# Performance work log

Measured on AMD Instinct MI355X. Metric: run time of the kernel, lower is better.

The kernel has to match this reference:

```python
import jax, jax.numpy as jnp
import numpy as np

NUM_HEADS = 12


def setup_inputs() -> dict:
    key = jax.random.key(0)
    ks = jax.random.split(key, 9)
    B, T, C = 4, 2048, 768
    s = 1.0 / np.sqrt(C)
    return {
        "x": jax.random.normal(ks[0], (B, T, C), dtype=jnp.float32),
        "wq": jax.random.normal(ks[1], (C, C), dtype=jnp.float32) * s,
        "bq": jnp.zeros((C,), dtype=jnp.float32),
        "wk": jax.random.normal(ks[2], (C, C), dtype=jnp.float32) * s,
        "bk": jnp.zeros((C,), dtype=jnp.float32),
        "wv": jax.random.normal(ks[3], (C, C), dtype=jnp.float32) * s,
        "bv": jnp.zeros((C,), dtype=jnp.float32),
        "wo": jax.random.normal(ks[4], (C, C), dtype=jnp.float32) * s,
        "bo": jnp.zeros((C,), dtype=jnp.float32),
    }


def reference(x, wq, bq, wk, bk, wv, bv, wo, bo):
    B, T, C = x.shape
    H = NUM_HEADS
    D = C // H
    scale = D ** -0.5
    # projections: weights stored as [in, out] so y = x @ w + b
    q = (x @ wq + bq).reshape(B, T, H, D).transpose(0, 2, 1, 3)  # [B,H,T,D]
    k = (x @ wk + bk).reshape(B, T, H, D).transpose(0, 2, 1, 3)
    v = (x @ wv + bv).reshape(B, T, H, D).transpose(0, 2, 1, 3)
    scores = jnp.einsum("bhqd,bhkd->bhqk", q, k) * scale  # [B,H,T,T]
    probs = jax.nn.softmax(scores, axis=-1)
    out = jnp.einsum("bhqk,bhkd->bhqd", probs, v)  # [B,H,T,D]
    out = out.transpose(0, 2, 1, 3).reshape(B, T, C)
    return out @ wo + bo
```

## Files before the change

kernel.cpp:

```cpp
#include <hip/hip_runtime.h>
#include <math.h>

#define NB 4
#define T_SEQ 2048
#define C_DIM 768
#define NH 12
#define HD 64
#define M_TOK (NB * T_SEQ)
#define NE ((size_t)M_TOK * C_DIM)
#define WE ((size_t)C_DIM * C_DIM)
#define QSCALE 0.18033688011112042f

typedef short bf16x8 __attribute__((ext_vector_type(8)));
typedef float f32x4 __attribute__((ext_vector_type(4)));
typedef unsigned short u16x4 __attribute__((ext_vector_type(4)));
typedef unsigned short u16x8 __attribute__((ext_vector_type(8)));
typedef unsigned short ushort_t;

__device__ __forceinline__ unsigned short f2bf(float x) {
    unsigned u = __float_as_uint(x);
    u += 0x7FFFu + ((u >> 16) & 1u);
    return (unsigned short)(u >> 16);
}
__device__ __forceinline__ float bf2f(unsigned short h) {
    return __uint_as_float(((unsigned)h) << 16);
}
__device__ __forceinline__ int sw128(int row, int bytecol) {
    return row * 128 + (bytecol ^ ((row & 7) << 4));
}
__device__ __forceinline__ void gload16(const ushort_t* gp, ushort_t* lp) {
    __builtin_amdgcn_global_load_lds(
        (const __attribute__((address_space(1))) unsigned int*)(const void*)gp,
        (__attribute__((address_space(3))) unsigned int*)(void*)lp, 16, 0, 0);
}

__global__ __launch_bounds__(256) void prep(
    const float* __restrict__ X,
    const float* __restrict__ wq, const float* __restrict__ wk,
    const float* __restrict__ wv, const float* __restrict__ wo,
    ushort_t* __restrict__ XH, ushort_t* __restrict__ Wbase)
{
    __shared__ float T[64][65];
    const int tid = threadIdx.x;
    const int bid = blockIdx.x;

    if (bid < 3072) {
        const size_t i = ((size_t)bid * 256 + tid) * 8;
        const float4 f0 = *(const float4*)&X[i];
        const float4 f1 = *(const float4*)&X[i + 4];
        const float xs[8] = {f0.x, f0.y, f0.z, f0.w, f1.x, f1.y, f1.z, f1.w};
        u16x8 h;
        #pragma unroll
        for (int j = 0; j < 8; ++j) h[j] = f2bf(xs[j]);
        *(u16x8*)&XH[i] = h;
        return;
    }

    const int r_ = bid - 3072;
    const int z = r_ / 144;
    const int rem = r_ % 144;
    const int ti = rem / 12, nj = rem % 12;
    const float* W = (z == 0) ? wq : (z == 1) ? wk : (z == 2) ? wv : wo;
    ushort_t* TH = Wbase + (size_t)z * 2 * WE;
    ushort_t* TL = TH + WE;
    {
        const int r = tid >> 2, cq = (tid & 3) * 16;
        #pragma unroll
        for (int j = 0; j < 4; ++j) {
            const float4 f = *(const float4*)&W[(size_t)(ti * 64 + r) * C_DIM + nj * 64 + cq + j * 4];
            T[r][cq + j * 4 + 0] = f.x;
            T[r][cq + j * 4 + 1] = f.y;
            T[r][cq + j * 4 + 2] = f.z;
            T[r][cq + j * 4 + 3] = f.w;
        }
    }
    __syncthreads();
    {
        const int n = tid >> 2, kq = (tid & 3) * 16;
        u16x8 h0, h1, l0, l1;
        #pragma unroll
        for (int j = 0; j < 8; ++j) {
            float v = T[kq + j][n];
            unsigned short hh = f2bf(v);
            h0[j] = hh; l0[j] = f2bf(v - bf2f(hh));
            v = T[kq + 8 + j][n];
            hh = f2bf(v);
            h1[j] = hh; l1[j] = f2bf(v - bf2f(hh));
        }
        const size_t o = (size_t)(nj * 64 + n) * C_DIM + ti * 64 + kq;
        *(u16x8*)&TH[o] = h0; *(u16x8*)&TH[o + 8] = h1;
        *(u16x8*)&TL[o] = l0; *(u16x8*)&TL[o + 8] = l1;
    }
}

__global__ __launch_bounds__(256, 4) void gemm_qkv(
    const ushort_t* __restrict__ XH,
    const ushort_t* __restrict__ WQH, const ushort_t* __restrict__ WKH,
    const ushort_t* __restrict__ WVH,
    const float* __restrict__ bq, const float* __restrict__ bk,
    const float* __restrict__ bv,
    ushort_t* __restrict__ Qo, ushort_t* __restrict__ Ko, ushort_t* __restrict__ VTo)
{
    __shared__ ushort_t TA[2][128 * 32];
    __shared__ ushort_t TB[2][128 * 32];

    const int tid = threadIdx.x, lane = tid & 63, w = tid >> 6;
    const int l15 = lane & 15, g = lane >> 4;
    const int wr = w >> 1, wc = w & 1;

    int bid = (int)blockIdx.x;
    bid = (bid & 7) * 144 + (bid >> 3);
    const int bm = bid / 18, bn = bid % 18;
    const int wsel = bn / 6, bnw = bn % 6;

    const ushort_t* BH = (wsel == 0) ? WQH : (wsel == 1) ? WKH : WVH;
    const float* bias = (wsel == 0) ? bq : (wsel == 1) ? bk : bv;

    f32x4 acc[4][4];
    #pragma unroll
    for (int m = 0; m < 4; ++m)
        #pragma unroll
        for (int n = 0; n < 4; ++n) acc[m][n] = (f32x4){0.f, 0.f, 0.f, 0.f};

    auto stage = [&](int buf, int k0) {
        #pragma unroll
        for (int p = 0; p < 4; ++p) {
            const int cb = 256 * p + 64 * w;
            const int c  = cb + lane;
            const int row = (c & 511) >> 2;
            const int slot = (c & 3) ^ ((row >> 1) & 3);
            if (cb < 512)
                gload16(XH + ((size_t)bm * 128 + row) * C_DIM + k0 + slot * 8,
                        &TA[buf][(cb & 511) * 8]);
            else
                gload16(BH + ((size_t)bnw * 128 + row) * C_DIM + k0 + slot * 8,
                        &TB[buf][(cb & 511) * 8]);
        }
    };

    stage(0, 0);
    int cur = 0;
    if (wsel < 2) {
        for (int k0 = 0; k0 < C_DIM; k0 += 32) {
            __syncthreads();
            if (k0 + 32 < C_DIM) stage(cur ^ 1, k0 + 32);
            bf16x8 ah[4], bh_[4];
            #pragma unroll
            for (int m = 0; m < 4; ++m) {
                const int r = 64 * wr + 16 * m + l15;
                const int off = r * 64 + ((g ^ ((r >> 1) & 3)) << 4);
                ah[m] = *(const bf16x8*)((const char*)TA[cur] + off);
            }
            #pragma unroll
            for (int n = 0; n < 4; ++n) {
                const int r = 64 * wc + 16 * n + l15;
                const int off = r * 64 + ((g ^ ((r >> 1) & 3)) << 4);
                bh_[n] = *(const bf16x8*)((const char*)TB[cur] + off);
            }
            #pragma unroll
            for (int m = 0; m < 4; ++m)
                #pragma unroll
                for (int n = 0; n < 4; ++n)
                    acc[m][n] = __builtin_amdgcn_mfma_f32_16x16x32_bf16(bh_[n], ah[m], acc[m][n], 0, 0, 0);
            cur ^= 1;
        }
        const float oscale = (wsel == 0) ? QSCALE : 1.0f;
        ushort_t* OH = (wsel == 0) ? Qo : Ko;
        #pragma unroll
        for (int n = 0; n < 4; ++n) {
            const int colw0 = bnw * 128 + 64 * wc + 16 * n + 4 * g;
            const float4 bv4 = *(const float4*)&bias[colw0];
            const float bvr[4] = {bv4.x, bv4.y, bv4.z, bv4.w};
            const int h = colw0 >> 6, d0 = colw0 & 63;
            #pragma unroll
            for (int m = 0; m < 4; ++m) {
                const int t = bm * 128 + 64 * wr + 16 * m + l15;
                const int b = t >> 11, tt = t & (T_SEQ - 1);
                u16x4 ph;
                #pragma unroll
                for (int r = 0; r < 4; ++r)
                    ph[r] = f2bf((acc[m][n][r] + bvr[r]) * oscale);
                *(u16x4*)&OH[(((size_t)b * NH + h) * T_SEQ + tt) * HD + d0] = ph;
            }
        }
    } else {
        for (int k0 = 0; k0 < C_DIM; k0 += 32) {
            __syncthreads();
            if (k0 + 32 < C_DIM) stage(cur ^ 1, k0 + 32);
            bf16x8 ah[4], bh_[4];
            #pragma unroll
            for (int m = 0; m < 4; ++m) {
                const int r = 64 * wr + 16 * m + l15;
                const int off = r * 64 + ((g ^ ((r >> 1) & 3)) << 4);
                ah[m] = *(const bf16x8*)((const char*)TA[cur] + off);
            }
            #pragma unroll
            for (int n = 0; n < 4; ++n) {
                const int r = 64 * wc + 16 * n + l15;
                const int off = r * 64 + ((g ^ ((r >> 1) & 3)) << 4);
                bh_[n] = *(const bf16x8*)((const char*)TB[cur] + off);
            }
            #pragma unroll
            for (int m = 0; m < 4; ++m)
                #pragma unroll
                for (int n = 0; n < 4; ++n)
                    acc[m][n] = __builtin_amdgcn_mfma_f32_16x16x32_bf16(ah[m], bh_[n], acc[m][n], 0, 0, 0);
            cur ^= 1;
        }
        #pragma unroll
        for (int n = 0; n < 4; ++n) {
            const int colw = bnw * 128 + 64 * wc + 16 * n + l15;
            const float bv_ = bias[colw];
            const int h = colw >> 6, d = colw & 63;
            #pragma unroll
            for (int m = 0; m < 4; ++m) {
                const int row0 = bm * 128 + 64 * wr + 16 * m + 4 * g;
                u16x4 ph;
                #pragma unroll
                for (int r = 0; r < 4; ++r) ph[r] = f2bf(acc[m][n][r] + bv_);
                const int b = row0 >> 11, t0 = row0 & (T_SEQ - 1);
                *(u16x4*)&VTo[(((size_t)b * NH + h) * HD + d) * T_SEQ + t0] = ph;
            }
        }
    }
}

__global__ __launch_bounds__(256, 4) void gemm_out(
    const ushort_t* __restrict__ AB,
    const ushort_t* __restrict__ BH, const ushort_t* __restrict__ BL,
    const float* __restrict__ bias, float* __restrict__ OutF)
{
    __shared__ ushort_t TA[2][128 * 32];
    __shared__ ushort_t TB[2][2][64 * 32];

    const int tid = threadIdx.x, lane = tid & 63, w = tid >> 6;
    const int l15 = lane & 15, g = lane >> 4;
    const int wr = w >> 1, wc = w & 1;

    int bid = (int)blockIdx.x;
    bid = (bid & 7) * 96 + (bid >> 3);
    const int bm = bid / 12, bn = bid % 12;

    f32x4 acc[4][2];
    #pragma unroll
    for (int m = 0; m < 4; ++m)
        #pragma unroll
        for (int n = 0; n < 2; ++n) acc[m][n] = (f32x4){0.f, 0.f, 0.f, 0.f};

    auto stage = [&](int buf, int k0) {
        #pragma unroll
        for (int p = 0; p < 4; ++p) {
            const int c = w + 4 * p;
            if (c < 8) {
                const int row = c * 16 + (lane >> 2);
                const int slot = (lane & 3) ^ ((row >> 1) & 3);
                gload16(AB + ((size_t)bm * 128 + row) * C_DIM + k0 + slot * 8,
                        &TA[buf][c * 512]);
            } else {
                const int t_ = (c - 8) >> 2;
                const int cc = c & 3;
                const int row = cc * 16 + (lane >> 2);
                const int slot = (lane & 3) ^ ((row >> 1) & 3);
                const ushort_t* src = (t_ ? BL : BH) + ((size_t)bn * 64 + row) * C_DIM + k0 + slot * 8;
                gload16(src, &TB[buf][t_][cc * 512]);
            }
        }
    };

    stage(0, 0);
    int cur = 0;
    for (int k0 = 0; k0 < C_DIM; k0 += 32) {
        __syncthreads();
        if (k0 + 32 < C_DIM) stage(cur ^ 1, k0 + 32);

        bf16x8 a_[4], bh_[2], bl_[2];
        #pragma unroll
        for (int m = 0; m < 4; ++m) {
            const int r = 64 * wr + 16 * m + l15;
            const int off = r * 64 + ((g ^ ((r >> 1) & 3)) << 4);
            a_[m] = *(const bf16x8*)((const char*)TA[cur] + off);
        }
        #pragma unroll
        for (int n = 0; n < 2; ++n) {
            const int r = 32 * wc + 16 * n + l15;
            const int off = r * 64 + ((g ^ ((r >> 1) & 3)) << 4);
            bh_[n] = *(const bf16x8*)((const char*)TB[cur][0] + off);
            bl_[n] = *(const bf16x8*)((const char*)TB[cur][1] + off);
        }
        #pragma unroll
        for (int m = 0; m < 4; ++m)
            #pragma unroll
            for (int n = 0; n < 2; ++n) {
                acc[m][n] = __builtin_amdgcn_mfma_f32_16x16x32_bf16(a_[m], bh_[n], acc[m][n], 0, 0, 0);
                acc[m][n] = __builtin_amdgcn_mfma_f32_16x16x32_bf16(a_[m], bl_[n], acc[m][n], 0, 0, 0);
            }
        cur ^= 1;
    }

    #pragma unroll
    for (int n = 0; n < 2; ++n) {
        const int col = bn * 64 + 32 * wc + 16 * n + l15;
        const float bv = bias[col];
        #pragma unroll
        for (int m = 0; m < 4; ++m) {
            const int row0 = bm * 128 + 64 * wr + 16 * m + 4 * g;
            #pragma unroll
            for (int r = 0; r < 4; ++r)
                OutF[(size_t)(row0 + r) * C_DIM + col] = acc[m][n][r] + bv;
        }
    }
}

__global__ __launch_bounds__(256, 3) void attn_fuse8(
    const ushort_t* __restrict__ QB, const ushort_t* __restrict__ KB,
    const ushort_t* __restrict__ VTB, ushort_t* __restrict__ ABo)
{
    __shared__ ushort_t Ks[2][64 * 64];
    __shared__ ushort_t Vt[2][64 * 64];
    __shared__ ushort_t Pm[4][32 * 64];

    const int tid = threadIdx.x, lane = tid & 63, w = tid >> 6;
    const int l15 = lane & 15, g = lane >> 4;

    int bid = (int)blockIdx.x;
    bid = (bid & 7) * 96 + (bid >> 3);
    const int bh = bid >> 4, qt = bid & 15;
    const int b = bh / NH, h = bh % NH;

    bf16x8 qf0[2], qf1[2];
    #pragma unroll
    for (int kc = 0; kc < 2; ++kc) {
        const size_t base = ((size_t)bh * T_SEQ + qt * 128 + 32 * w + l15) * HD + kc * 32 + g * 8;
        qf0[kc] = *(const bf16x8*)&QB[base];
        qf1[kc] = *(const bf16x8*)&QB[base + (size_t)16 * HD];
    }

    bf16x8 onesf;
    #pragma unroll
    for (int j = 0; j < 8; ++j) onesf[j] = (short)0x3F80;

    f32x4 o0[4], o1[4];
    #pragma unroll
    for (int nd = 0; nd < 4; ++nd) {
        o0[nd] = (f32x4){0.f, 0.f, 0.f, 0.f};
        o1[nd] = (f32x4){0.f, 0.f, 0.f, 0.f};
    }
    f32x4 ol0 = (f32x4){0.f, 0.f, 0.f, 0.f};
    f32x4 ol1 = (f32x4){0.f, 0.f, 0.f, 0.f};

    const ushort_t* kb = KB + (size_t)bh * T_SEQ * HD;
    const ushort_t* vb = VTB + (size_t)bh * HD * T_SEQ;
    const int swz = (l15 & 7) << 4;

    const ushort_t *gK0, *gK1, *gV0, *gV1;
    {
        const int c0 = w * 64 + lane;
        const int r0 = c0 >> 3;
        const int cb0 = ((c0 & 7) * 16) ^ ((r0 & 7) << 4);
        gK0 = kb + (size_t)r0 * HD + (cb0 >> 1);
        gV0 = vb + (size_t)r0 * T_SEQ + (cb0 >> 1);
        const int c1 = c0 + 256;
        const int r1 = c1 >> 3;
        const int cb1 = ((c1 & 7) * 16) ^ ((r1 & 7) << 4);
        gK1 = kb + (size_t)r1 * HD + (cb1 >> 1);
        gV1 = vb + (size_t)r1 * T_SEQ + (cb1 >> 1);
    }
    ushort_t* dK0 = &Ks[0][w * 512];
    ushort_t* dK1 = &Ks[0][2048 + w * 512];
    ushort_t* dV0 = &Vt[0][w * 512];
    ushort_t* dV1 = &Vt[0][2048 + w * 512];

    auto stage = [&](int buf) {
        const int o = buf * 4096;
        gload16(gK0, dK0 + o); gK0 += (size_t)64 * HD;
        gload16(gK1, dK1 + o); gK1 += (size_t)64 * HD;
        gload16(gV0, dV0 + o); gV0 += 64;
        gload16(gV1, dV1 + o); gV1 += 64;
    };

    stage(0);
    int cur = 0;
    for (int kt = 0; kt < T_SEQ; kt += 64) {
        __syncthreads();
        if (kt + 64 < T_SEQ) stage(cur ^ 1);

        const char* ksb = (const char*)Ks + cur * 8192;
        const char* vtb = (const char*)Vt + cur * 8192;

        f32x4 s0[4], s1[4];
        #pragma unroll
        for (int nb = 0; nb < 4; ++nb) {
            s0[nb] = (f32x4){0.f, 0.f, 0.f, 0.f};
            s1[nb] = (f32x4){0.f, 0.f, 0.f, 0.f};
        }
        __builtin_amdgcn_s_setprio(1);
        #pragma unroll
        for (int kc = 0; kc < 2; ++kc)
            #pragma unroll
            for (int nb = 0; nb < 4; ++nb) {
                const bf16x8 kf = *(const bf16x8*)(ksb + sw128(16 * nb + l15, kc * 64 + g * 16));
                s0[nb] = __builtin_amdgcn_mfma_f32_16x16x32_bf16(kf, qf0[kc], s0[nb], 0, 0, 0);
                s1[nb] = __builtin_amdgcn_mfma_f32_16x16x32_bf16(kf, qf1[kc], s1[nb], 0, 0, 0);
            }
        __builtin_amdgcn_s_setprio(0);

        #pragma unroll
        for (int nb = 0; nb < 4; ++nb) {
            const float a0 = __builtin_amdgcn_exp2f(s0[nb][0]);
            const float a1 = __builtin_amdgcn_exp2f(s0[nb][1]);
            const float a2 = __builtin_amdgcn_exp2f(s0[nb][2]);
            const float a3 = __builtin_amdgcn_exp2f(s0[nb][3]);
            const unsigned dwa0 = __builtin_amdgcn_perm(
                __float_as_uint(a1), __float_as_uint(a0), 0x07060302u);
            const unsigned dwa1 = __builtin_amdgcn_perm(
                __float_as_uint(a3), __float_as_uint(a2), 0x07060302u);
            *(uint2*)((char*)Pm[w] + l15 * 128 + ((32 * nb + 8 * g) ^ swz)) =
                make_uint2(dwa0, dwa1);

            const float b0 = __builtin_amdgcn_exp2f(s1[nb][0]);
            const float b1 = __builtin_amdgcn_exp2f(s1[nb][1]);
            const float b2 = __builtin_amdgcn_exp2f(s1[nb][2]);
            const float b3 = __builtin_amdgcn_exp2f(s1[nb][3]);
            const unsigned dwb0 = __builtin_amdgcn_perm(
                __float_as_uint(b1), __float_as_uint(b0), 0x07060302u);
            const unsigned dwb1 = __builtin_amdgcn_perm(
                __float_as_uint(b3), __float_as_uint(b2), 0x07060302u);
            *(uint2*)((char*)Pm[w] + (16 + l15) * 128 + ((32 * nb + 8 * g) ^ swz)) =
                make_uint2(dwb0, dwb1);
        }

        #pragma unroll
        for (int kc2 = 0; kc2 < 2; ++kc2) {
            const bf16x8 pb0 = *(const bf16x8*)((const char*)Pm[w] + l15 * 128 + ((kc2 * 64 + g * 16) ^ swz));
            const bf16x8 pb1 = *(const bf16x8*)((const char*)Pm[w] + (16 + l15) * 128 + ((kc2 * 64 + g * 16) ^ swz));
            __builtin_amdgcn_s_setprio(1);
            #pragma unroll
            for (int nd = 0; nd < 4; ++nd) {
                const bf16x8 vf = *(const bf16x8*)(vtb + sw128(16 * nd + l15, kc2 * 64 + g * 16));
                o0[nd] = __builtin_amdgcn_mfma_f32_16x16x32_bf16(vf, pb0, o0[nd], 0, 0, 0);
                o1[nd] = __builtin_amdgcn_mfma_f32_16x16x32_bf16(vf, pb1, o1[nd], 0, 0, 0);
            }
            ol0 = __builtin_amdgcn_mfma_f32_16x16x32_bf16(onesf, pb0, ol0, 0, 0, 0);
            ol1 = __builtin_amdgcn_mfma_f32_16x16x32_bf16(onesf, pb1, ol1, 0, 0, 0);
            __builtin_amdgcn_s_setprio(0);
        }
        cur ^= 1;
    }

    const float inv0 = 1.0f / ol0[0];
    const float inv1 = 1.0f / ol1[0];
    const int t0 = qt * 128 + 32 * w + l15;
    #pragma unroll
    for (int nd = 0; nd < 4; ++nd) {
        u16x4 h0_, h1_;
        #pragma unroll
        for (int r = 0; r < 4; ++r) {
            h0_[r] = f2bf(o0[nd][r] * inv0);
            h1_[r] = f2bf(o1[nd][r] * inv1);
        }
        const size_t col = h * HD + 16 * nd + 4 * g;
        *(u16x4*)&ABo[((size_t)b * T_SEQ + t0) * C_DIM + col] = h0_;
        *(u16x4*)&ABo[((size_t)b * T_SEQ + t0 + 16) * C_DIM + col] = h1_;
    }
}

extern "C" void kernel_launch(void* const* d_in, const int* in_sizes, int n_in,
                              void* d_out, int out_size, void* d_ws, size_t ws_size,
                              hipStream_t stream)
{
    const float* x  = (const float*)d_in[0];
    const float* wq = (const float*)d_in[1];
    const float* bq = (const float*)d_in[2];
    const float* wk = (const float*)d_in[3];
    const float* bk = (const float*)d_in[4];
    const float* wv = (const float*)d_in[5];
    const float* bv = (const float*)d_in[6];
    const float* wo = (const float*)d_in[7];
    const float* bo = (const float*)d_in[8];

    ushort_t* Wbase = (ushort_t*)d_ws;
    ushort_t* WQ_H = Wbase;
    ushort_t* WK_H = Wbase + 2 * WE;
    ushort_t* WV_H = Wbase + 4 * WE;
    ushort_t* WO_H = Wbase + 6 * WE;
    ushort_t* WO_L = WO_H + WE;
    ushort_t* X_H  = Wbase + 8 * WE;
    ushort_t* K_B  = X_H + 2 * NE;
    ushort_t* VT_B = K_B + NE;
    ushort_t* Q_B = (ushort_t*)d_out;
    ushort_t* A_B = X_H;

    const dim3 blk(256);

    prep<<<3648, blk, 0, stream>>>(x, wq, wk, wv, wo, X_H, Wbase);

    gemm_qkv<<<1152, blk, 0, stream>>>(X_H, WQ_H, WK_H, WV_H,
                                       bq, bk, bv, Q_B, K_B, VT_B);

    attn_fuse8<<<768, blk, 0, stream>>>(Q_B, K_B, VT_B, A_B);

    gemm_out<<<768, blk, 0, stream>>>(A_B, WO_H, WO_L, bo, (float*)d_out);
}
```

Baseline: 147.9 us.

## Load 128-key K/V tiles per barrier pair and vectorize output GEMM stores

The attention kernel drops its double-buffered prefetch, which overlapped loading the next 64-key tile with compute on the current one. It now loads two 64-key K/V halves at once between two barriers and processes both halves from shared memory, halving the number of sync rounds per key sweep. Global load latency is no longer hidden behind compute, so progress now relies on other resident blocks to cover the gaps. Separately, the output GEMM swaps its MFMA operands so each lane holds four consecutive columns, which allows float4 bias loads and float4 output stores instead of scalar strided writes.

```diff
diff --git a/kernel.cpp b/kernel.cpp
--- a/kernel.cpp
+++ b/kernel.cpp
@@ -291,27 +291,30 @@
         for (int m = 0; m < 4; ++m)
             #pragma unroll
             for (int n = 0; n < 2; ++n) {
-                acc[m][n] = __builtin_amdgcn_mfma_f32_16x16x32_bf16(a_[m], bh_[n], acc[m][n], 0, 0, 0);
-                acc[m][n] = __builtin_amdgcn_mfma_f32_16x16x32_bf16(a_[m], bl_[n], acc[m][n], 0, 0, 0);
+                acc[m][n] = __builtin_amdgcn_mfma_f32_16x16x32_bf16(bh_[n], a_[m], acc[m][n], 0, 0, 0);
+                acc[m][n] = __builtin_amdgcn_mfma_f32_16x16x32_bf16(bl_[n], a_[m], acc[m][n], 0, 0, 0);
             }
         cur ^= 1;
     }
 
     #pragma unroll
     for (int n = 0; n < 2; ++n) {
-        const int col = bn * 64 + 32 * wc + 16 * n + l15;
-        const float bv = bias[col];
+        const int col0 = bn * 64 + 32 * wc + 16 * n + 4 * g;
+        const float4 bv4 = *(const float4*)&bias[col0];
         #pragma unroll
         for (int m = 0; m < 4; ++m) {
-            const int row0 = bm * 128 + 64 * wr + 16 * m + 4 * g;
-            #pragma unroll
-            for (int r = 0; r < 4; ++r)
-                OutF[(size_t)(row0 + r) * C_DIM + col] = acc[m][n][r] + bv;
-        }
-    }
-}
-
-__global__ __launch_bounds__(256, 3) void attn_fuse8(
+            const int token = bm * 128 + 64 * wr + 16 * m + l15;
+            float4 v;
+            v.x = acc[m][n][0] + bv4.x;
+            v.y = acc[m][n][1] + bv4.y;
+            v.z = acc[m][n][2] + bv4.z;
+            v.w = acc[m][n][3] + bv4.w;
+            *(float4*)&OutF[(size_t)token * C_DIM + col0] = v;
+        }
+    }
+}
+
+__global__ __launch_bounds__(256, 3) void attn_fuse9(
     const ushort_t* __restrict__ QB, const ushort_t* __restrict__ KB,
     const ushort_t* __restrict__ VTB, ushort_t* __restrict__ ABo)
 {
@@ -370,81 +373,83 @@
     ushort_t* dV0 = &Vt[0][w * 512];
     ushort_t* dV1 = &Vt[0][2048 + w * 512];
 
-    auto stage = [&](int buf) {
-        const int o = buf * 4096;
-        gload16(gK0, dK0 + o); gK0 += (size_t)64 * HD;
-        gload16(gK1, dK1 + o); gK1 += (size_t)64 * HD;
-        gload16(gV0, dV0 + o); gV0 += 64;
-        gload16(gV1, dV1 + o); gV1 += 64;
-    };
-
-    stage(0);
-    int cur = 0;
-    for (int kt = 0; kt < T_SEQ; kt += 64) {
+    for (int kt = 0; kt < T_SEQ; kt += 128) {
         __syncthreads();
-        if (kt + 64 < T_SEQ) stage(cur ^ 1);
-
-        const char* ksb = (const char*)Ks + cur * 8192;
-        const char* vtb = (const char*)Vt + cur * 8192;
-
-        f32x4 s0[4], s1[4];
-        #pragma unroll
-        for (int nb = 0; nb < 4; ++nb) {
-            s0[nb] = (f32x4){0.f, 0.f, 0.f, 0.f};
-            s1[nb] = (f32x4){0.f, 0.f, 0.f, 0.f};
-        }
-        __builtin_amdgcn_s_setprio(1);
-        #pragma unroll
-        for (int kc = 0; kc < 2; ++kc)
+        gload16(gK0, dK0);
+        gload16(gK1, dK1);
+        gload16(gV0, dV0);
+        gload16(gV1, dV1);
+        gload16(gK0 + (size_t)64 * HD, dK0 + 4096);
+        gload16(gK1 + (size_t)64 * HD, dK1 + 4096);
+        gload16(gV0 + 64, dV0 + 4096);
+        gload16(gV1 + 64, dV1 + 4096);
+        gK0 += (size_t)128 * HD; gK1 += (size_t)128 * HD;
+        gV0 += 128; gV1 += 128;
+        __syncthreads();
+
+        #pragma unroll
+        for (int half = 0; half < 2; ++half) {
+            const char* ksb = (const char*)Ks[half];
+            const char* vtb = (const char*)Vt[half];
+
+            f32x4 s0[4], s1[4];
             #pragma unroll
             for (int nb = 0; nb < 4; ++nb) {
-                const bf16x8 kf = *(const bf16x8*)(ksb + sw128(16 * nb + l15, kc * 64 + g * 16));
-                s0[nb] = __builtin_amdgcn_mfma_f32_16x16x32_bf16(kf, qf0[kc], s0[nb], 0, 0, 0);
-                s1[nb] = __builtin_amdgcn_mfma_f32_16x16x32_bf16(kf, qf1[kc], s1[nb], 0, 0, 0);
-            }
-        __builtin_amdgcn_s_setprio(0);
-
-        #pragma unroll
-        for (int nb = 0; nb < 4; ++nb) {
-            const float a0 = __builtin_amdgcn_exp2f(s0[nb][0]);
-            const float a1 = __builtin_amdgcn_exp2f(s0[nb][1]);
-            const float a2 = __builtin_amdgcn_exp2f(s0[nb][2]);
-            const float a3 = __builtin_amdgcn_exp2f(s0[nb][3]);
-            const unsigned dwa0 = __builtin_amdgcn_perm(
-                __float_as_uint(a1), __float_as_uint(a0), 0x07060302u);
-            const unsigned dwa1 = __builtin_amdgcn_perm(
-                __float_as_uint(a3), __float_as_uint(a2), 0x07060302u);
-            *(uint2*)((char*)Pm[w] + l15 * 128 + ((32 * nb + 8 * g) ^ swz)) =
-                make_uint2(dwa0, dwa1);
-
-            const float b0 = __builtin_amdgcn_exp2f(s1[nb][0]);
-            const float b1 = __builtin_amdgcn_exp2f(s1[nb][1]);
-            const float b2 = __builtin_amdgcn_exp2f(s1[nb][2]);
-            const float b3 = __builtin_amdgcn_exp2f(s1[nb][3]);
-            const unsigned dwb0 = __builtin_amdgcn_perm(
-                __float_as_uint(b1), __float_as_uint(b0), 0x07060302u);
-            const unsigned dwb1 = __builtin_amdgcn_perm(
-                __float_as_uint(b3), __float_as_uint(b2), 0x07060302u);
-            *(uint2*)((char*)Pm[w] + (16 + l15) * 128 + ((32 * nb + 8 * g) ^ swz)) =
-                make_uint2(dwb0, dwb1);
-        }
-
-        #pragma unroll
-        for (int kc2 = 0; kc2 < 2; ++kc2) {
-            const bf16x8 pb0 = *(const bf16x8*)((const char*)Pm[w] + l15 * 128 + ((kc2 * 64 + g * 16) ^ swz));
-            const bf16x8 pb1 = *(const bf16x8*)((const char*)Pm[w] + (16 + l15) * 128 + ((kc2 * 64 + g * 16) ^ swz));
+                s0[nb] = (f32x4){0.f, 0.f, 0.f, 0.f};
+                s1[nb] = (f32x4){0.f, 0.f, 0.f, 0.f};
+            }
             __builtin_amdgcn_s_setprio(1);
             #pragma unroll
-            for (int nd = 0; nd < 4; ++nd) {
-                const bf16x8 vf = *(const bf16x8*)(vtb + sw128(16 * nd + l15, kc2 * 64 + g * 16));
-                o0[nd] = __builtin_amdgcn_mfma_f32_16x16x32_bf16(vf, pb0, o0[nd], 0, 0, 0);
-                o1[nd] = __builtin_amdgcn_mfma_f32_16x16x32_bf16(vf, pb1, o1[nd], 0, 0, 0);
-            }
-            ol0 = __builtin_amdgcn_mfma_f32_16x16x32_bf16(onesf, pb0, ol0, 0, 0, 0);
-            ol1 = __builtin_amdgcn_mfma_f32_16x16x32_bf16(onesf, pb1, ol1, 0, 0, 0);
+            for (int kc = 0; kc < 2; ++kc)
+                #pragma unroll
+                for (int nb = 0; nb < 4; ++nb) {
+                    const bf16x8 kf = *(const bf16x8*)(ksb + sw128(16 * nb + l15, kc * 64 + g * 16));
+                    s0[nb] = __builtin_amdgcn_mfma_f32_16x16x32_bf16(kf, qf0[kc], s0[nb], 0, 0, 0);
+                    s1[nb] = __builtin_amdgcn_mfma_f32_16x16x32_bf16(kf, qf1[kc], s1[nb], 0, 0, 0);
+                }
             __builtin_amdgcn_s_setprio(0);
-        }
-        cur ^= 1;
+
+            #pragma unroll
+            for (int nb = 0; nb < 4; ++nb) {
+                const float a0 = __builtin_amdgcn_exp2f(s0[nb][0]);
+                const float a1 = __builtin_amdgcn_exp2f(s0[nb][1]);
+                const float a2 = __builtin_amdgcn_exp2f(s0[nb][2]);
+                const float a3 = __builtin_amdgcn_exp2f(s0[nb][3]);
+                const unsigned dwa0 = __builtin_amdgcn_perm(
+                    __float_as_uint(a1), __float_as_uint(a0), 0x07060302u);
+                const unsigned dwa1 = __builtin_amdgcn_perm(
+                    __float_as_uint(a3), __float_as_uint(a2), 0x07060302u);
+                *(uint2*)((char*)Pm[w] + l15 * 128 + ((32 * nb + 8 * g) ^ swz)) =
+                    make_uint2(dwa0, dwa1);
+
+                const float b0 = __builtin_amdgcn_exp2f(s1[nb][0]);
+                const float b1 = __builtin_amdgcn_exp2f(s1[nb][1]);
+                const float b2 = __builtin_amdgcn_exp2f(s1[nb][2]);
+                const float b3 = __builtin_amdgcn_exp2f(s1[nb][3]);
+                const unsigned dwb0 = __builtin_amdgcn_perm(
+                    __float_as_uint(b1), __float_as_uint(b0), 0x07060302u);
+                const unsigned dwb1 = __builtin_amdgcn_perm(
+                    __float_as_uint(b3), __float_as_uint(b2), 0x07060302u);
+                *(uint2*)((char*)Pm[w] + (16 + l15) * 128 + ((32 * nb + 8 * g) ^ swz)) =
+                    make_uint2(dwb0, dwb1);
+            }
+
+            #pragma unroll
+            for (int kc2 = 0; kc2 < 2; ++kc2) {
+                const bf16x8 pb0 = *(const bf16x8*)((const char*)Pm[w] + l15 * 128 + ((kc2 * 64 + g * 16) ^ swz));
+                const bf16x8 pb1 = *(const bf16x8*)((const char*)Pm[w] + (16 + l15) * 128 + ((kc2 * 64 + g * 16) ^ swz));
+                __builtin_amdgcn_s_setprio(1);
+                #pragma unroll
+                for (int nd = 0; nd < 4; ++nd) {
+                    const bf16x8 vf = *(const bf16x8*)(vtb + sw128(16 * nd + l15, kc2 * 64 + g * 16));
+                    o0[nd] = __builtin_amdgcn_mfma_f32_16x16x32_bf16(vf, pb0, o0[nd], 0, 0, 0);
+                    o1[nd] = __builtin_amdgcn_mfma_f32_16x16x32_bf16(vf, pb1, o1[nd], 0, 0, 0);
+                }
+                ol0 = __builtin_amdgcn_mfma_f32_16x16x32_bf16(onesf, pb0, ol0, 0, 0, 0);
+                ol1 = __builtin_amdgcn_mfma_f32_16x16x32_bf16(onesf, pb1, ol1, 0, 0, 0);
+                __builtin_amdgcn_s_setprio(0);
+            }
+        }
     }
 
     const float inv0 = 1.0f / ol0[0];
@@ -497,7 +502,7 @@
     gemm_qkv<<<1152, blk, 0, stream>>>(X_H, WQ_H, WK_H, WV_H,
                                        bq, bk, bv, Q_B, K_B, VT_B);
 
-    attn_fuse8<<<768, blk, 0, stream>>>(Q_B, K_B, VT_B, A_B);
+    attn_fuse9<<<768, blk, 0, stream>>>(Q_B, K_B, VT_B, A_B);
 
     gemm_out<<<768, blk, 0, stream>>>(A_B, WO_H, WO_L, bo, (float*)d_out);
 }
```

Result: no change. 149.1 us (+0.8%).
